# Optimization experiments

Measured on AMD Instinct MI355X. Metric: run time of the kernel, lower is better.

## Reference

```python
import jax, jax.numpy as jnp
import numpy as np

S_FACTOR = 2          # scale_factor
GRID = 64             # coarse grid side -> M = 64^3 coarse voxels
C_IN = 32
C_MID = 32
C_OUT = 256


def setup_inputs() -> dict:
    key = jax.random.key(0)
    k1, k2, k3 = jax.random.split(key, 3)
    s = S_FACTOR
    S = s ** 3
    M = GRID ** 3
    # coarse voxel coords in canonical (lexicographic) order
    r = jnp.arange(GRID)
    ci, cj, ck = jnp.meshgrid(r, r, r, indexing='ij')
    coarse = jnp.stack([ci.ravel(), cj.ravel(), ck.ravel()], axis=-1)  # (M, 3)
    lo = jnp.arange(s)
    li, lj, lk = jnp.meshgrid(lo, lo, lo, indexing='ij')
    local = jnp.stack([li.ravel(), lj.ravel(), lk.ravel()], axis=-1)   # (S, 3)
    # fine voxel coords: every coarse voxel fully occupied -> N = M*S
    ijk = (coarse[:, None, :] * s + local[None, :, :]).reshape(M * S, 3).astype(jnp.int32)
    # ijk_to_index on the coarse grid (precomputed grid lookup, int constant)
    down_index = jnp.repeat(jnp.arange(M, dtype=jnp.int32), S)
    in_data = jax.random.normal(k1, (M * S, C_IN), dtype=jnp.float32)
    W_mid = jax.random.normal(k2, (C_IN, C_MID), dtype=jnp.float32) / np.sqrt(C_IN).astype(np.float32)
    W_out = jax.random.normal(k3, (C_MID * S, C_OUT), dtype=jnp.float32) / np.sqrt(C_MID * S).astype(np.float32)
    return {"in_data": in_data, "W_mid": W_mid, "W_out": W_out,
            "ijk": ijk, "down_index": down_index, "num_coarse": M}


def reference(in_data, W_mid, W_out, ijk, down_index, num_coarse):
    s = S_FACTOR
    S = s ** 3
    # middle_proj (LinearFVDB, bias=False)
    x = in_data @ W_mid                                   # (N, C_mid)
    C = x.shape[1]
    # local coordinate within the s^3 block (floor division; ijk >= 0 here)
    down_ijk = ijk // s
    local = ijk - down_ijk * s                            # (N, 3) in [0, s)
    local_index = local[:, 0] * (s * s) + local[:, 1] * s + local[:, 2]
    flat_idx = down_index.astype(jnp.int32) * S + local_index.astype(jnp.int32)
    # scatter_add into zero buffer (mapping is a unique permutation)
    flat_target = jnp.zeros((num_coarse * S, C), dtype=x.dtype).at[flat_idx].add(x)
    down_data = flat_target.reshape(num_coarse, S * C)    # (M, S*C)
    # out_proj (LinearFVDB, bias=False)
    return down_data @ W_out                              # (M, C_out)
```

## Files before the change

kernel.cpp:

```cpp
#include <hip/hip_runtime.h>
#include <hip/hip_bf16.h>


typedef short bf16x8 __attribute__((ext_vector_type(8)));
typedef float f32x4 __attribute__((ext_vector_type(4)));

__device__ __forceinline__ unsigned short f2bf(float f) {
    union { float f; unsigned u; } x; x.f = f;
    unsigned u = x.u;
    u += 0x7fffu + ((u >> 16) & 1u);
    return (unsigned short)(u >> 16);
}

__global__ void build_wf(const float* __restrict__ Wmid,
                         const float* __restrict__ Wout,
                         unsigned short* __restrict__ Wt) {
    const int o = blockIdx.x;
    const int k = threadIdx.x;
    const int s = k >> 5;
    const int j = k & 31;
    float acc = 0.f;
#pragma unroll
    for (int c = 0; c < 32; ++c)
        acc += Wmid[j * 32 + c] * Wout[(s * 32 + c) * 256 + o];
    Wt[o * 256 + k] = f2bf(acc);
}

__global__ void build_inv(const int* __restrict__ ijk,
                          const int* __restrict__ down,
                          int* __restrict__ inv, int n) {
    int i = blockIdx.x * 256 + threadIdx.x;
    if (i < n) {
        int a = ijk[3 * i], b = ijk[3 * i + 1], c = ijk[3 * i + 2];
        int ls = ((a & 1) << 2) | ((b & 1) << 1) | (c & 1);
        inv[down[i] * 8 + ls] = i;
    }
}

__global__ __launch_bounds__(256) void gemm_fused(
    const float* __restrict__ A,
    const int* __restrict__ inv,
    const unsigned short* __restrict__ Wt,
    float* __restrict__ out)
{
    __shared__ int invS[512];
    __shared__ __align__(16) unsigned short Abuf[64 * 32];
    __shared__ __align__(16) unsigned short Bbuf[256 * 32];

    const int t = threadIdx.x;
    const long m0 = (long)blockIdx.x * 64;

    invS[t]       = inv[m0 * 8 + t];
    invS[256 + t] = inv[m0 * 8 + 256 + t];

    const int wave = t >> 6;
    const int lane = t & 63;
    const int q    = lane >> 4;
    const int r16  = lane & 15;

    f32x4 acc[4][4];
#pragma unroll
    for (int i = 0; i < 4; ++i)
#pragma unroll
        for (int j = 0; j < 4; ++j)
            acc[i][j] = (f32x4){0.f, 0.f, 0.f, 0.f};

    __syncthreads();

    for (int kb = 0; kb < 8; ++kb) {
#pragma unroll
        for (int i = 0; i < 2; ++i) {
            int flat = t + i * 256;
            int row  = flat >> 3;
            int seg  = flat & 7;
            long g   = invS[row * 8 + kb];
            const float4 v = *(const float4*)(A + g * 32 + seg * 4);
            ushort4 b;
            b.x = f2bf(v.x); b.y = f2bf(v.y); b.z = f2bf(v.z); b.w = f2bf(v.w);
            *(ushort4*)(&Abuf[row * 32 + seg * 4]) = b;
        }
#pragma unroll
        for (int i = 0; i < 4; ++i) {
            int c = t + i * 256;
            int o = c >> 2;
            int seg = c & 3;
            *(int4*)(&Bbuf[o * 32 + seg * 8]) =
                *(const int4*)(Wt + (long)o * 256 + kb * 32 + seg * 8);
        }
        __syncthreads();

        bf16x8 af[4], bfr[4];
#pragma unroll
        for (int mt = 0; mt < 4; ++mt)
            af[mt] = *(const bf16x8*)(&Abuf[(mt * 16 + r16) * 32 + q * 8]);
#pragma unroll
        for (int nt = 0; nt < 4; ++nt)
            bfr[nt] = *(const bf16x8*)(&Bbuf[(wave * 64 + nt * 16 + r16) * 32 + q * 8]);
#pragma unroll
        for (int mt = 0; mt < 4; ++mt)
#pragma unroll
            for (int nt = 0; nt < 4; ++nt)
                acc[mt][nt] = __builtin_amdgcn_mfma_f32_16x16x32_bf16(
                    af[mt], bfr[nt], acc[mt][nt], 0, 0, 0);
        __syncthreads();
    }

#pragma unroll
    for (int mt = 0; mt < 4; ++mt)
#pragma unroll
        for (int nt = 0; nt < 4; ++nt)
#pragma unroll
            for (int rg = 0; rg < 4; ++rg) {
                int row = mt * 16 + q * 4 + rg;
                int col = wave * 64 + nt * 16 + r16;
                out[(m0 + row) * 256 + col] = acc[mt][nt][rg];
            }
}

extern "C" void kernel_launch(void* const* d_in, const int* in_sizes, int n_in,
                              void* d_out, int out_size, void* d_ws, size_t ws_size,
                              hipStream_t stream) {
    const float* in_data = (const float*)d_in[0];
    const float* W_mid   = (const float*)d_in[1];
    const float* W_out   = (const float*)d_in[2];
    const int*   ijk     = (const int*)d_in[3];
    const int*   down    = (const int*)d_in[4];

    const int Nf = in_sizes[0] / 32;
    const int M  = Nf / 8;

    unsigned short* Wt = (unsigned short*)d_ws;
    int* inv = (int*)((char*)d_ws + 131072);

    build_wf<<<256, 256, 0, stream>>>(W_mid, W_out, Wt);
    build_inv<<<(Nf + 255) / 256, 256, 0, stream>>>(ijk, down, inv, Nf);
    gemm_fused<<<M / 64, 256, 0, stream>>>(in_data, inv, Wt, (float*)d_out);
}
```

Baseline: 524.8 us.

## Load GEMM fragments directly from global memory, drop LDS staging and barriers

The fused gather-GEMM no longer stages A and B tiles through shared memory. Each wave loads its own A fragments straight from the gathered input rows, converting them to bf16 in registers, and reads B fragments directly from the precomputed weight matrix. This removes the per-iteration barriers and LDS round trips, and the K loop is fully unrolled. The cost is that all four waves redundantly load the same A rows from global or cache, and output stores become nontemporal.

```diff
diff --git a/kernel.cpp b/kernel.cpp
--- a/kernel.cpp
+++ b/kernel.cpp
@@ -44,8 +44,6 @@
     float* __restrict__ out)
 {
     __shared__ int invS[512];
-    __shared__ __align__(16) unsigned short Abuf[64 * 32];
-    __shared__ __align__(16) unsigned short Bbuf[256 * 32];
 
     const int t = threadIdx.x;
     const long m0 = (long)blockIdx.x * 64;
@@ -67,42 +65,33 @@
 
     __syncthreads();
 
+    const unsigned short* Wbase = Wt + (long)(wave * 64 + r16) * 256 + q * 8;
+
+#pragma unroll
     for (int kb = 0; kb < 8; ++kb) {
+        bf16x8 af[4], bfr[4];
 #pragma unroll
-        for (int i = 0; i < 2; ++i) {
-            int flat = t + i * 256;
-            int row  = flat >> 3;
-            int seg  = flat & 7;
-            long g   = invS[row * 8 + kb];
-            const float4 v = *(const float4*)(A + g * 32 + seg * 4);
-            ushort4 b;
-            b.x = f2bf(v.x); b.y = f2bf(v.y); b.z = f2bf(v.z); b.w = f2bf(v.w);
-            *(ushort4*)(&Abuf[row * 32 + seg * 4]) = b;
+        for (int mt = 0; mt < 4; ++mt) {
+            long g = invS[(mt * 16 + r16) * 8 + kb];
+            const float* ap = A + g * 32 + q * 8;
+            const float4 v0 = *(const float4*)(ap);
+            const float4 v1 = *(const float4*)(ap + 4);
+            union { bf16x8 v; __hip_bfloat162 h[4]; } u;
+            u.h[0] = __float22bfloat162_rn(make_float2(v0.x, v0.y));
+            u.h[1] = __float22bfloat162_rn(make_float2(v0.z, v0.w));
+            u.h[2] = __float22bfloat162_rn(make_float2(v1.x, v1.y));
+            u.h[3] = __float22bfloat162_rn(make_float2(v1.z, v1.w));
+            af[mt] = u.v;
         }
 #pragma unroll
-        for (int i = 0; i < 4; ++i) {
-            int c = t + i * 256;
-            int o = c >> 2;
-            int seg = c & 3;
-            *(int4*)(&Bbuf[o * 32 + seg * 8]) =
-                *(const int4*)(Wt + (long)o * 256 + kb * 32 + seg * 8);
-        }
-        __syncthreads();
-
-        bf16x8 af[4], bfr[4];
-#pragma unroll
-        for (int mt = 0; mt < 4; ++mt)
-            af[mt] = *(const bf16x8*)(&Abuf[(mt * 16 + r16) * 32 + q * 8]);
-#pragma unroll
         for (int nt = 0; nt < 4; ++nt)
-            bfr[nt] = *(const bf16x8*)(&Bbuf[(wave * 64 + nt * 16 + r16) * 32 + q * 8]);
+            bfr[nt] = *(const bf16x8*)(Wbase + (long)nt * 16 * 256 + kb * 32);
 #pragma unroll
         for (int mt = 0; mt < 4; ++mt)
 #pragma unroll
             for (int nt = 0; nt < 4; ++nt)
                 acc[mt][nt] = __builtin_amdgcn_mfma_f32_16x16x32_bf16(
                     af[mt], bfr[nt], acc[mt][nt], 0, 0, 0);
-        __syncthreads();
     }
 
 #pragma unroll
@@ -113,7 +102,8 @@
             for (int rg = 0; rg < 4; ++rg) {
                 int row = mt * 16 + q * 4 + rg;
                 int col = wave * 64 + nt * 16 + r16;
-                out[(m0 + row) * 256 + col] = acc[mt][nt][rg];
+                __builtin_nontemporal_store(acc[mt][nt][rg],
+                                            out + (m0 + row) * 256 + col);
             }
 }
 
```

Result: slower. 622.0 us (+18.5%).
